# Kernel optimization log

Measured on AMD Instinct MI355X. Metric: run time of the kernel, lower is better.

The kernel has to match this reference:

```python
import jax, jax.numpy as jnp
import numpy as np

B, L, H, N = 50, 1024, 512, 512
DT = 1e-3          # step from source
N_DEQ = 8          # fixed-point iterations for the implicit (DEQ) layer
EPS = 1e-5


def setup_inputs():
    key = jax.random.key(0)
    ks = jax.random.split(key, 8)
    s = lambda k, shape: jax.random.normal(k, shape, jnp.float32) * 0.02
    return dict(
        x=jax.random.normal(ks[0], (B, L, 1), jnp.float32),
        W_emb=s(ks[1], (1, H)), b_emb=jnp.zeros((H,), jnp.float32),
        C_re=s(ks[2], (6, H, N)), C_im=s(ks[3], (6, H, N)),
        D=jnp.ones((6, H), jnp.float32),
        ln_g=jnp.ones((6, H), jnp.float32), ln_b=jnp.zeros((6, H), jnp.float32),
        W_feed=s(ks[4], (H, H)), b_feed=jnp.zeros((H,), jnp.float32),
        W_fc=s(ks[5], (H, 10)), b_fc=jnp.zeros((10,), jnp.float32),
    )


def _kernels(C_re, C_im):
    # S4D-Lin init for A (shared across channels in this untrained reference):
    # A_n = -1/2 + i*pi*n. ZOH discretization with step DT.
    n = jnp.arange(N)
    A = -0.5 + 1j * jnp.pi * n                       # [N]
    dA = jnp.exp(DT * A)                              # [N]
    dB = (dA - 1.0) / A                               # [N] (B = 1)
    l = jnp.arange(L)
    V = jnp.exp(DT * A[:, None] * l[None, :])         # [N, L] Vandermonde dA^l
    C = C_re.astype(jnp.complex64) + 1j * C_im.astype(jnp.complex64)  # [6,H,N]
    K = 2.0 * jnp.real(jnp.einsum('khn,nl->khl', C * dB, V))          # [6,H,L]
    return K.astype(jnp.float32)


def _conv(u, K):
    # causal convolution of u [B,L,H] with per-channel kernel K [H,L]
    Uf = jnp.fft.rfft(u, n=2 * L, axis=1)             # [B, L+1, H]
    Kf = jnp.fft.rfft(K.T, n=2 * L, axis=0)           # [L+1, H]
    y = jnp.fft.irfft(Uf * Kf[None], n=2 * L, axis=1)[:, :L]
    return y


def _ln(x, g, b):
    m = jnp.mean(x, axis=-1, keepdims=True)
    v = jnp.var(x, axis=-1, keepdims=True)
    return (x - m) * jax.lax.rsqrt(v + EPS) * g + b


def _s4d_block(u, K, D, g, b, act, skip):
    v = _ln(u, g, b)
    y = act(_conv(v, K) + v * D)                      # SSM + skip-through D
    return y + u if skip else y


def _deq(x, Ks, Ds, gs, bs, W_feed, b_feed):
    # implicit layer: fixed-point of z = f(z; x), f = 3 stacked S4D blocks
    # + gelu + gelu feedforward, with input injection (skip=False, dropout=0)
    def f(z):
        h = z + x
        for i in range(3):
            h = _s4d_block(h, Ks[i], Ds[i], gs[i], bs[i], jnp.tanh, False)
        h = jax.nn.gelu(h)
        return jax.nn.gelu(h @ W_feed + b_feed)
    z = jnp.zeros_like(x)
    for _ in range(N_DEQ - 1):
        z = f(z)
    z_new = f(z)
    loss = jnp.mean((z_new - z) ** 2)                 # fixed-point residual
    return z_new, loss


def reference(x, W_emb, b_emb, C_re, C_im, D, ln_g, ln_b, W_feed, b_feed, W_fc, b_fc):
    K = _kernels(C_re, C_im)                          # [6,H,L]
    r = x @ W_emb + b_emb                             # [B,L,H]
    y = r
    for i in range(3):                                # 3 explicit S4D blocks
        y = _s4d_block(y, K[i], D[i], ln_g[i], ln_b[i], jnp.tanh, True)
    h, loss = _deq(y, K[3:], D[3:], ln_g[3:], ln_b[3:], W_feed, b_feed)
    logits = jnp.mean(h, axis=1) @ W_fc + b_fc        # [B,10]
    return logits, loss, h, jnp.int32(N_DEQ)
```

## Files before the change

### kernel.cpp

```cpp
#include <hip/hip_runtime.h>
#include <hip/hip_bf16.h>

typedef __hip_bfloat16 bf16;
typedef unsigned short u16;
typedef unsigned int u32;
typedef __attribute__((ext_vector_type(8))) short short8;
typedef __attribute__((ext_vector_type(4))) float f32x4;

#define B_ 50
#define L_ 1024
#define H_ 512
#define N_ 512
#define BL_ 51200
#define HBL_ 26214400
#define KROW_ 1088
#define PI_F 3.14159265358979323846f
#define MARK_BF16 0x3F803F80u
#define KRSW_ 1112
#define CONV_LDS_BYTES 151040

__device__ __forceinline__ float u2f(u16 u){ union{u32 i; float f;} v; v.i = ((u32)u)<<16; return v.f; }
__device__ __forceinline__ u16  f2u(float x){ bf16 b = __float2bfloat16(x); return *(u16*)&b; }

__device__ __forceinline__ float ld_in(const void* p, int i, bool bff){
  if (bff){ u16 v = ((const u16*)p)[i]; union{u32 a; float f;} u; u.a = ((u32)v)<<16; return u.f; }
  return ((const float*)p)[i];
}

__device__ __forceinline__ float gelu_f(float x){
  float t = tanhf(0.7978845608028654f*(x + 0.044715f*x*x*x));
  return 0.5f*x*(1.0f + t);
}

__global__ __launch_bounds__(256) void kV(float* __restrict__ Vre, float* __restrict__ Vim){
  int idx = blockIdx.x*256 + threadIdx.x;
  int n = idx >> 10, l = idx & 1023;
  int ph = (n*l) % 2000;
  float ang = (float)ph * (PI_F/1000.f);
  float mag = expf(-5e-4f*(float)l);
  float s, c;
  sincosf(ang, &s, &c);
  Vre[idx] = mag*c;
  Vim[idx] = mag*s;
}

__global__ __launch_bounds__(256) void kX(const u32* __restrict__ mk,
                                          const void* __restrict__ Cre, const void* __restrict__ Cim,
                                          float* __restrict__ Xre, float* __restrict__ Xim){
  const bool bff = (*mk == MARK_BF16);
  int idx = blockIdx.x*256 + threadIdx.x;
  int n = idx & (N_-1);
  float ar = -0.5f, ai = PI_F*(float)n;
  float ex = expf(-5e-4f);
  float s, c;
  sincosf(1e-3f*ai, &s, &c);
  float dre = ex*c - 1.f;
  float dim = ex*s;
  float inv = 1.f/(ar*ar + ai*ai);
  float dBre = (dre*ar + dim*ai)*inv;
  float dBim = (dim*ar - dre*ai)*inv;
  float cr = ld_in(Cre, idx, bff), ci = ld_in(Cim, idx, bff);
  Xre[idx] = cr*dBre - ci*dBim;
  Xim[idx] = cr*dBim + ci*dBre;
}

__global__ __launch_bounds__(256) void kK(const float* __restrict__ Xre, const float* __restrict__ Xim,
                                          const float* __restrict__ Vre, const float* __restrict__ Vim,
                                          u16* __restrict__ Kbp){
  __shared__ float sxr[16*128], sxi[16*128];
  int kh0 = blockIdx.x*16;
  int l0 = blockIdx.y*512 + threadIdx.x;
  float accA[16], accB[16];
  #pragma unroll
  for (int t=0;t<16;++t){ accA[t]=0.f; accB[t]=0.f; }
  for (int nc=0; nc<4; ++nc){
    if (nc) __syncthreads();
    #pragma unroll
    for (int q=0;q<8;++q){
      int e = q*256 + threadIdx.x;
      int r = e >> 7, c = e & 127;
      sxr[e] = Xre[(kh0+r)*N_ + nc*128 + c];
      sxi[e] = Xim[(kh0+r)*N_ + nc*128 + c];
    }
    __syncthreads();
    for (int n4=0;n4<32;++n4){
      int nb = (nc*128 + n4*4)*L_ + l0;
      float vrA[4], viA[4], vrB[4], viB[4];
      #pragma unroll
      for (int k=0;k<4;++k){
        vrA[k] = Vre[nb + k*L_];       viA[k] = Vim[nb + k*L_];
        vrB[k] = Vre[nb + k*L_ + 256]; viB[k] = Vim[nb + k*L_ + 256];
      }
      #pragma unroll
      for (int t=0;t<16;++t){
        f32x4 xr = *(const f32x4*)&sxr[t*128 + n4*4];
        f32x4 xi = *(const f32x4*)&sxi[t*128 + n4*4];
        float a = accA[t], b = accB[t];
        #pragma unroll
        for (int k=0;k<4;++k){
          a += xr[k]*vrA[k] - xi[k]*viA[k];
          b += xr[k]*vrB[k] - xi[k]*viB[k];
        }
        accA[t] = a; accB[t] = b;
      }
    }
  }
  #pragma unroll
  for (int t=0;t<16;++t){
    Kbp[(kh0+t)*KROW_ + 64 + l0]       = f2u(2.f*accA[t]);
    Kbp[(kh0+t)*KROW_ + 64 + l0 + 256] = f2u(2.f*accB[t]);
  }
  if (blockIdx.y == 0 && threadIdx.x < 64){
    #pragma unroll
    for (int t=0;t<16;++t) Kbp[(kh0+t)*KROW_ + threadIdx.x] = 0;
  }
}

__global__ __launch_bounds__(256) void kWb(const u32* __restrict__ mk,
                                           const void* __restrict__ W, u16* __restrict__ Wbt){
  const bool bff = (*mk == MARK_BF16);
  int idx = blockIdx.x*256 + threadIdx.x;
  int k = idx >> 9, m = idx & 511;
  Wbt[m*512 + k] = f2u(ld_in(W, k*512 + m, bff));
}

__global__ __launch_bounds__(256) void kEmbed(const u32* __restrict__ mk,
                                              const void* __restrict__ x, const void* __restrict__ W,
                                              const void* __restrict__ be, u16* __restrict__ out){
  const bool bff = (*mk == MARK_BF16);
  int t = blockIdx.x*256 + threadIdx.x;
  int e = t*4;
  int h = e / BL_;
  int col = e - h*BL_;
  float w = ld_in(W, h, bff), bb = ld_in(be, h, bff);
  ushort4 o;
  o.x = f2u(ld_in(x, col+0, bff)*w + bb);
  o.y = f2u(ld_in(x, col+1, bff)*w + bb);
  o.z = f2u(ld_in(x, col+2, bff)*w + bb);
  o.w = f2u(ld_in(x, col+3, bff)*w + bb);
  *(ushort4*)(out + e) = o;
}

__global__ __launch_bounds__(256) void kZero(uint4* __restrict__ Z, float* __restrict__ lossAcc){
  int t = blockIdx.x*256 + threadIdx.x;
  Z[t] = make_uint4(0u,0u,0u,0u);
  if (t == 0) *lossAcc = 0.f;
}

__global__ __launch_bounds__(256) void kLN2(const u32* __restrict__ mk,
                                            const u16* __restrict__ U, const u16* __restrict__ U2,
                                            const void* __restrict__ g, const void* __restrict__ bb,
                                            int off, u16* __restrict__ Vout){
  const bool bff = (*mk == MARK_BF16);
  __shared__ float rs[32][64], rq[32][64], ms[64], rr[64], gs[512], bs[512];
  int c8 = threadIdx.x & 7;
  int ty = threadIdx.x >> 3;
  int colb = blockIdx.x*64 + c8*8;
  for (int i = threadIdx.x; i < 512; i += 256){
    gs[i] = ld_in(g, off+i, bff);
    bs[i] = ld_in(bb, off+i, bff);
  }
  float s8[8], q8[8];
  #pragma unroll
  for (int j=0;j<8;++j){ s8[j]=0.f; q8[j]=0.f; }
  for (int p=0;p<16;++p){
    int h = ty + p*32;
    uint4 uv = *(const uint4*)(U + (size_t)h*BL_ + colb);
    const u16* pu = (const u16*)&uv;
    float xv[8];
    #pragma unroll
    for (int j=0;j<8;++j) xv[j] = u2f(pu[j]);
    if (U2){
      uint4 uv2 = *(const uint4*)(U2 + (size_t)h*BL_ + colb);
      const u16* p2 = (const u16*)&uv2;
      #pragma unroll
      for (int j=0;j<8;++j) xv[j] += u2f(p2[j]);
    }
    #pragma unroll
    for (int j=0;j<8;++j){ s8[j] += xv[j]; q8[j] += xv[j]*xv[j]; }
  }
  *(f32x4*)&rs[ty][c8*8]   = (f32x4){s8[0],s8[1],s8[2],s8[3]};
  *(f32x4*)&rs[ty][c8*8+4] = (f32x4){s8[4],s8[5],s8[6],s8[7]};
  *(f32x4*)&rq[ty][c8*8]   = (f32x4){q8[0],q8[1],q8[2],q8[3]};
  *(f32x4*)&rq[ty][c8*8+4] = (f32x4){q8[4],q8[5],q8[6],q8[7]};
  __syncthreads();
  if (threadIdx.x < 64){
    int c = threadIdx.x;
    float st = 0.f, qt = 0.f;
    #pragma unroll 8
    for (int t2=0;t2<32;++t2){ st += rs[t2][c]; qt += rq[t2][c]; }
    float mean = st*(1.f/512.f);
    float var  = qt*(1.f/512.f) - mean*mean;
    ms[c] = mean;
    rr[c] = rsqrtf(var + 1e-5f);
  }
  __syncthreads();
  float mean8[8], rstd8[8];
  #pragma unroll
  for (int j=0;j<8;++j){ mean8[j] = ms[c8*8+j]; rstd8[j] = rr[c8*8+j]; }
  for (int p=0;p<16;++p){
    int h = ty + p*32;
    uint4 uv = *(const uint4*)(U + (size_t)h*BL_ + colb);
    const u16* pu = (const u16*)&uv;
    float xv[8];
    #pragma unroll
    for (int j=0;j<8;++j) xv[j] = u2f(pu[j]);
    if (U2){
      uint4 uv2 = *(const uint4*)(U2 + (size_t)h*BL_ + colb);
      const u16* p2 = (const u16*)&uv2;
      #pragma unroll
      for (int j=0;j<8;++j) xv[j] += u2f(p2[j]);
    }
    float gv = gs[h], bv = bs[h];
    union { uint4 v; u16 s[8]; } ob;
    #pragma unroll
    for (int j=0;j<8;++j) ob.s[j] = f2u((xv[j]-mean8[j])*rstd8[j]*gv + bv);
    *(uint4*)(Vout + (size_t)h*BL_ + colb) = ob.v;
  }
}

__global__ __launch_bounds__(512, 2) void kConvM(const u32* __restrict__ mk,
                                              const u16* __restrict__ V, const u16* __restrict__ Kb,
                                              const void* __restrict__ Dv, int dOff,
                                              const u16* __restrict__ U,
                                              u16* __restrict__ Y, int skip, int doGelu){
  extern __shared__ u16 lds[];
  u16* sV  = lds;
  u16* sKR = lds + 65536;
  u16* sKt = lds + 65536 + 8*KRSW_;
  const bool bff = (*mk == MARK_BF16);
  int h = blockIdx.x;
  int tid = threadIdx.x;
  const u16* Kbh = Kb + h*KROW_;
  for (int s = tid; s < 1088; s += 512) sKt[s] = Kbh[s];
  __syncthreads();
  #pragma unroll
  for (int p = 0; p < 8; ++p){
    for (int s = tid; s < KRSW_; s += 512){
      int idx = 1087 - s - p;
      sKR[p*KRSW_ + s] = (idx >= 0) ? sKt[idx] : (u16)0;
    }
  }
  {
    const u16* Vh = V + (size_t)h*(B_*L_);
    #pragma unroll
    for (int q = 0; q < 16; ++q){
      int chunk = q*512 + tid;
      int r = chunk >> 7;
      int c16 = chunk & 127;
      uint4 dval = *(const uint4*)(Vh + r*L_ + c16*8);
      u32 byte = ((u32)r << 11) + ((u32)c16 << 4);
      byte ^= ((u32)(r & 7) << 4);
      *(uint4*)((char*)sV + byte) = dval;
    }
  }
  __syncthreads();
  int wv = tid >> 6, lane = tid & 63;
  int nl = lane & 15, quad = lane >> 4;
  float Dh = ld_in(Dv, dOff + h, bff);
  #pragma unroll 1
  for (int cc = 0; cc < 2; ++cc){
    int c_out = cc ? (15 - wv) : wv;
    f32x4 acc[4][4];
    #pragma unroll
    for (int mt=0;mt<4;++mt){
      #pragma unroll
      for (int nt=0;nt<4;++nt) acc[mt][nt] = (f32x4){0.f,0.f,0.f,0.f};
    }
    for (int ci = 0; ci <= c_out; ++ci){
      int d = c_out - ci;
      short8 a0[4], a1[4], b0[4], b1[4];
      #pragma unroll
      for (int mt=0;mt<4;++mt){
        int r = mt*16 + nl;
        u32 msk = (u32)(r & 7) << 4;
        u32 base = ((u32)r << 11) + (u32)((ci*64 + quad*8) << 1);
        a0[mt] = *(const short8*)((const char*)sV + (base ^ msk));
        a1[mt] = *(const short8*)((const char*)sV + ((base + 64u) ^ msk));
      }
      #pragma unroll
      for (int nt=0;nt<4;++nt){
        int i = nt*16 + nl;
        int t0 = 1023 - d*64 - i + quad*8;
        const u16* bp = sKR + (t0 & 7)*KRSW_ + (t0 & ~7);
        b0[nt] = *(const short8*)bp;
        b1[nt] = *(const short8*)(bp + 32);
      }
      #pragma unroll
      for (int mt=0;mt<4;++mt){
        #pragma unroll
        for (int nt=0;nt<4;++nt){
          acc[mt][nt] = __builtin_amdgcn_mfma_f32_16x16x32_bf16(a0[mt], b0[nt], acc[mt][nt], 0,0,0);
          acc[mt][nt] = __builtin_amdgcn_mfma_f32_16x16x32_bf16(a1[mt], b1[nt], acc[mt][nt], 0,0,0);
        }
      }
    }
    #pragma unroll
    for (int mt=0;mt<4;++mt){
      #pragma unroll
      for (int reg=0;reg<4;++reg){
        int b = mt*16 + quad*4 + reg;
        if (b < B_){
          #pragma unroll
          for (int nt=0;nt<4;++nt){
            int col = c_out*64 + nt*16 + nl;
            u32 vb = (((u32)b << 11) + ((u32)col << 1)) ^ ((u32)(b & 7) << 4);
            float vv = u2f(*(const u16*)((const char*)sV + vb));
            size_t gi = (size_t)(h*B_ + b)*L_ + col;
            float y = tanhf(acc[mt][nt][reg] + vv*Dh);
            if (skip) y += u2f(U[gi]);
            if (doGelu) y = gelu_f(y);
            Y[gi] = f2u(y);
          }
        }
      }
    }
  }
}

__global__ __launch_bounds__(256) void kTY(const u16* __restrict__ Y, u16* __restrict__ Yt){
  __shared__ u16 st[64][68];
  int n0 = blockIdx.x*64, k0 = blockIdx.y*64;
  int tid = threadIdx.x;
  int r = tid >> 2, q = tid & 3;
  const u16* src = Y + (size_t)(k0 + r)*BL_ + n0 + q*16;
  #pragma unroll
  for (int c=0; c<4; ++c){
    ushort4 v = *(const ushort4*)(src + c*4);
    st[r][q*16 + c*4 + 0] = v.x;
    st[r][q*16 + c*4 + 1] = v.y;
    st[r][q*16 + c*4 + 2] = v.z;
    st[r][q*16 + c*4 + 3] = v.w;
  }
  __syncthreads();
  int i = tid & 63;
  int j0 = tid >> 6;
  for (int jj = j0; jj < 64; jj += 4){
    Yt[(size_t)(n0 + jj)*512 + k0 + i] = st[i][jj];
  }
}

__global__ __launch_bounds__(256) void kFFM(const u32* __restrict__ mk,
                                            const u16* __restrict__ Ytg, const u16* __restrict__ Wbt,
                                            const void* __restrict__ bias, u16* Zout,
                                            const u16* Zold, float* __restrict__ lossAcc, int doLoss){
  const bool bff = (*mk == MARK_BF16);
  int n0g = blockIdx.x*64, m0g = blockIdx.y*64;
  int tid = threadIdx.x;
  __shared__ __align__(16) u16 wa[64*72];
  __shared__ __align__(16) u16 yt[64*72];
  __shared__ float red[256];
  int wv = tid >> 6, lane = tid & 63;
  int nl = lane & 15, quad = lane >> 4;
  int n0 = wv*16;
  f32x4 acc[4];
  #pragma unroll
  for (int mt=0;mt<4;++mt) acc[mt] = (f32x4){0.f,0.f,0.f,0.f};
  int r = tid >> 2, c0 = (tid & 3) * 16;
  for (int kc=0; kc<8; ++kc){
    int k0g = kc*64;
    const u16* wp = Wbt + (m0g + r)*512 + k0g + c0;
    *(uint4*)&wa[r*72 + c0]     = *(const uint4*)wp;
    *(uint4*)&wa[r*72 + c0 + 8] = *(const uint4*)(wp + 8);
    const u16* yp = Ytg + (size_t)(n0g + r)*512 + k0g + c0;
    *(uint4*)&yt[r*72 + c0]     = *(const uint4*)yp;
    *(uint4*)&yt[r*72 + c0 + 8] = *(const uint4*)(yp + 8);
    __syncthreads();
    short8 bf0 = *(const short8*)&yt[(n0 + nl)*72 + quad*8];
    short8 bf1 = *(const short8*)&yt[(n0 + nl)*72 + 32 + quad*8];
    #pragma unroll
    for (int mt=0;mt<4;++mt){
      const u16* row = &wa[(mt*16 + nl)*72];
      short8 a0 = *(const short8*)&row[quad*8];
      short8 a1 = *(const short8*)&row[32 + quad*8];
      acc[mt] = __builtin_amdgcn_mfma_f32_16x16x32_bf16(a0, bf0, acc[mt], 0,0,0);
      acc[mt] = __builtin_amdgcn_mfma_f32_16x16x32_bf16(a1, bf1, acc[mt], 0,0,0);
    }
    __syncthreads();
  }
  float ls = 0.f;
  #pragma unroll
  for (int mt=0;mt<4;++mt){
    #pragma unroll
    for (int reg=0;reg<4;++reg){
      int m = m0g + mt*16 + quad*4 + reg;
      int col = n0g + n0 + nl;
      float val = gelu_f(acc[mt][reg] + ld_in(bias, m, bff));
      size_t zi = (size_t)m*BL_ + col;
      if (doLoss){ float d = val - u2f(Zold[zi]); ls += d*d; }
      Zout[zi] = f2u(val);
    }
  }
  if (doLoss){
    red[tid] = ls;
    __syncthreads();
    for (int off=128; off>0; off>>=1){
      if (tid < off) red[tid] += red[tid+off];
      __syncthreads();
    }
    if (tid==0) atomicAdd(lossAcc, red[0]);
  }
}

__global__ void kScalars(const float* __restrict__ lossAcc, float* __restrict__ outp){
  if (threadIdx.x == 0 && blockIdx.x == 0){
    outp[500] = *lossAcc * (1.f/26214400.f);
    outp[26214901] = 8.0f;
  }
}

__global__ __launch_bounds__(256) void kTrans(const u16* __restrict__ Z, float* __restrict__ out){
  __shared__ u16 st[64][68];
  int b = blockIdx.z, h0 = blockIdx.y*64, l0 = blockIdx.x*64;
  int tid = threadIdx.x;
  int r = tid >> 2, q = tid & 3;
  const u16* src = Z + ((h0+r)*B_ + b)*L_ + l0 + q*16;
  #pragma unroll
  for (int c=0; c<4; ++c){
    ushort4 v = *(const ushort4*)(src + c*4);
    st[r][q*16 + c*4 + 0] = v.x;
    st[r][q*16 + c*4 + 1] = v.y;
    st[r][q*16 + c*4 + 2] = v.z;
    st[r][q*16 + c*4 + 3] = v.w;
  }
  __syncthreads();
  int i = tid & 63;
  int j0 = tid >> 6;
  for (int jj = j0; jj < 64; jj += 4){
    out[(size_t)(b*L_ + l0 + jj)*H_ + h0 + i] = u2f(st[i][jj]);
  }
}

__global__ __launch_bounds__(256) void kMeanL(const u16* __restrict__ Z, float* __restrict__ Hb){
  int lane = threadIdx.x & 63;
  int ridx = blockIdx.x*4 + (threadIdx.x >> 6);
  const u16* row = Z + (size_t)ridx*L_;
  float s = 0.f;
  for (int ii=lane; ii<L_; ii+=64) s += u2f(row[ii]);
  for (int off=32; off>0; off>>=1) s += __shfl_down(s, off, 64);
  if (lane==0){
    int ho = ridx / B_, b = ridx - ho*B_;
    Hb[b*H_ + ho] = s*(1.f/1024.f);
  }
}

__global__ __launch_bounds__(256) void kLogits(const u32* __restrict__ mk,
                                               const float* __restrict__ Hb, const void* __restrict__ Wfc,
                                               const void* __restrict__ bfc, float* __restrict__ outp){
  const bool bff = (*mk == MARK_BF16);
  int t = blockIdx.x*256 + threadIdx.x;
  if (t < 500){
    int b = t/10, c = t - (t/10)*10;
    float s = ld_in(bfc, c, bff);
    for (int ho=0; ho<H_; ++ho) s += Hb[b*H_+ho]*ld_in(Wfc, ho*10+c, bff);
    outp[t] = s;
  }
}

extern "C" void kernel_launch(void* const* d_in, const int* in_sizes, int n_in,
                              void* d_out, int out_size, void* d_ws, size_t ws_size,
                              hipStream_t stream) {
  (void)in_sizes; (void)n_in; (void)out_size; (void)ws_size;
  const void* x      = d_in[0];
  const void* W_emb  = d_in[1];
  const void* b_emb  = d_in[2];
  const void* C_re   = d_in[3];
  const void* C_im   = d_in[4];
  const void* Dp     = d_in[5];
  const void* ln_g   = d_in[6];
  const void* ln_b   = d_in[7];
  const void* W_feed = d_in[8];
  const void* b_feed = d_in[9];
  const void* W_fc   = d_in[10];
  const void* b_fc   = d_in[11];
  const u32* mk = (const u32*)d_in[5];
  float* outp = (float*)d_out;

  static int s_attr = 0;
  if (!s_attr){
    hipFuncSetAttribute(reinterpret_cast<const void*>(kConvM),
                        hipFuncAttributeMaxDynamicSharedMemorySize, CONV_LDS_BYTES);
    s_attr = 1;
  }

  u16* Kbp = (u16*)d_ws;
  u16* Zb  = Kbp + 6*H_*KROW_;
  u16* T1  = Zb + HBL_;
  u16* T2  = T1 + HBL_;
  float* Hbar = (float*)(T2 + HBL_);
  float* lossAcc = Hbar + 25600;
  u16* Wbt = (u16*)(Hbar + 25604);
  u16* X0  = (u16*)d_out;
  u16* Yt  = X0 + HBL_;
  float* Vre = (float*)T1;
  float* Vim = Vre + N_*L_;
  float* Xre = Vim + N_*L_;
  float* Xim = Xre + 6*H_*N_;

  kV<<<2048, 256, 0, stream>>>(Vre, Vim);
  kX<<<6144, 256, 0, stream>>>(mk, C_re, C_im, Xre, Xim);
  kK<<<dim3(192,2), 256, 0, stream>>>(Xre, Xim, Vre, Vim, Kbp);
  kWb<<<1024, 256, 0, stream>>>(mk, W_feed, Wbt);

  kEmbed<<<25600, 256, 0, stream>>>(mk, x, W_emb, b_emb, X0);

  u16* cur = X0;
  u16* nxt = T2;
  for (int i=0;i<3;++i){
    kLN2<<<800,256,0,stream>>>(mk, cur, nullptr, ln_g, ln_b, i*H_, T1);
    kConvM<<<512, 512, CONV_LDS_BYTES, stream>>>(mk, T1, Kbp + i*H_*KROW_, Dp, i*H_, cur, nxt, 1, 0);
    u16* tmp = cur; cur = nxt; nxt = tmp;
  }
  u16* XINJ = cur;
  u16* BT   = nxt;

  kZero<<<12800, 256, 0, stream>>>((uint4*)Zb, lossAcc);
  for (int it=0; it<8; ++it){
    int last = (it == 7);
    kLN2<<<800,256,0,stream>>>(mk, Zb, XINJ, ln_g, ln_b, 3*H_, T1);
    kConvM<<<512, 512, CONV_LDS_BYTES, stream>>>(mk, T1, Kbp + 3*H_*KROW_, Dp, 3*H_, nullptr, BT, 0, 0);
    kLN2<<<800,256,0,stream>>>(mk, BT, nullptr, ln_g, ln_b, 4*H_, T1);
    kConvM<<<512, 512, CONV_LDS_BYTES, stream>>>(mk, T1, Kbp + 4*H_*KROW_, Dp, 4*H_, nullptr, BT, 0, 0);
    kLN2<<<800,256,0,stream>>>(mk, BT, nullptr, ln_g, ln_b, 5*H_, T1);
    kConvM<<<512, 512, CONV_LDS_BYTES, stream>>>(mk, T1, Kbp + 5*H_*KROW_, Dp, 5*H_, nullptr, BT, 0, 1);
    kTY<<<dim3(800,8),256,0,stream>>>(BT, Yt);
    kFFM<<<dim3(800,8),256,0,stream>>>(mk, Yt, Wbt, b_feed, Zb, Zb, lossAcc, last);
  }

  kMeanL<<<6400,256,0,stream>>>(Zb, Hbar);
  kScalars<<<1, 64, 0, stream>>>(lossAcc, outp);
  kTrans<<<dim3(16,8,50),256,0,stream>>>(Zb, outp + 501);
  kLogits<<<2,256,0,stream>>>(mk, Hbar, W_fc, b_fc, outp);
}
```

Baseline: 4.335 ms.

## Fuse transpose into feedforward GEMM, use fast tanh, shrink kernel-gen tiles

Removes the separate kTY transpose and the Yt buffer. The new kFF2 loads a 64-column slab of Y once into LDS, transposes it there, and loops over all 512 output rows while register-prefetching the weight tiles, so Y is read from global memory only once per column block. It also replaces tanhf with an exp-based tanh in the conv epilogue and in gelu, and halves the kK tile height to launch more blocks. The large LDS footprint per block lowers occupancy, and the fast tanh changes numerics slightly.

```diff
diff --git a/kernel.cpp b/kernel.cpp
--- a/kernel.cpp
+++ b/kernel.cpp
@@ -18,6 +18,8 @@
 #define MARK_BF16 0x3F803F80u
 #define KRSW_ 1112
 #define CONV_LDS_BYTES 151040
+#define FF_STR 584
+#define FF2_LDS_BYTES 153600
 
 __device__ __forceinline__ float u2f(u16 u){ union{u32 i; float f;} v; v.i = ((u32)u)<<16; return v.f; }
 __device__ __forceinline__ u16  f2u(float x){ bf16 b = __float2bfloat16(x); return *(u16*)&b; }
@@ -27,8 +29,15 @@
   return ((const float*)p)[i];
 }
 
+__device__ __forceinline__ float tanh_f(float x){
+  float ax = fabsf(x);
+  float e = __expf(2.f*ax);
+  float r = 1.f - 2.f/(e + 1.f);
+  return copysignf(r, x);
+}
+
 __device__ __forceinline__ float gelu_f(float x){
-  float t = tanhf(0.7978845608028654f*(x + 0.044715f*x*x*x));
+  float t = tanh_f(0.7978845608028654f*(x + 0.044715f*x*x*x));
   return 0.5f*x*(1.0f + t);
 }
 
@@ -67,16 +76,16 @@
 __global__ __launch_bounds__(256) void kK(const float* __restrict__ Xre, const float* __restrict__ Xim,
                                           const float* __restrict__ Vre, const float* __restrict__ Vim,
                                           u16* __restrict__ Kbp){
-  __shared__ float sxr[16*128], sxi[16*128];
-  int kh0 = blockIdx.x*16;
+  __shared__ float sxr[8*128], sxi[8*128];
+  int kh0 = blockIdx.x*8;
   int l0 = blockIdx.y*512 + threadIdx.x;
-  float accA[16], accB[16];
+  float accA[8], accB[8];
   #pragma unroll
-  for (int t=0;t<16;++t){ accA[t]=0.f; accB[t]=0.f; }
+  for (int t=0;t<8;++t){ accA[t]=0.f; accB[t]=0.f; }
   for (int nc=0; nc<4; ++nc){
     if (nc) __syncthreads();
     #pragma unroll
-    for (int q=0;q<8;++q){
+    for (int q=0;q<4;++q){
       int e = q*256 + threadIdx.x;
       int r = e >> 7, c = e & 127;
       sxr[e] = Xre[(kh0+r)*N_ + nc*128 + c];
@@ -92,7 +101,7 @@
         vrB[k] = Vre[nb + k*L_ + 256]; viB[k] = Vim[nb + k*L_ + 256];
       }
       #pragma unroll
-      for (int t=0;t<16;++t){
+      for (int t=0;t<8;++t){
         f32x4 xr = *(const f32x4*)&sxr[t*128 + n4*4];
         f32x4 xi = *(const f32x4*)&sxi[t*128 + n4*4];
         float a = accA[t], b = accB[t];
@@ -106,13 +115,13 @@
     }
   }
   #pragma unroll
-  for (int t=0;t<16;++t){
+  for (int t=0;t<8;++t){
     Kbp[(kh0+t)*KROW_ + 64 + l0]       = f2u(2.f*accA[t]);
     Kbp[(kh0+t)*KROW_ + 64 + l0 + 256] = f2u(2.f*accB[t]);
   }
   if (blockIdx.y == 0 && threadIdx.x < 64){
     #pragma unroll
-    for (int t=0;t<16;++t) Kbp[(kh0+t)*KROW_ + threadIdx.x] = 0;
+    for (int t=0;t<8;++t) Kbp[(kh0+t)*KROW_ + threadIdx.x] = 0;
   }
 }
 
@@ -307,7 +316,7 @@
             u32 vb = (((u32)b << 11) + ((u32)col << 1)) ^ ((u32)(b & 7) << 4);
             float vv = u2f(*(const u16*)((const char*)sV + vb));
             size_t gi = (size_t)(h*B_ + b)*L_ + col;
-            float y = tanhf(acc[mt][nt][reg] + vv*Dh);
+            float y = tanh_f(acc[mt][nt][reg] + vv*Dh);
             if (skip) y += u2f(U[gi]);
             if (doGelu) y = gelu_f(y);
             Y[gi] = f2u(y);
@@ -318,83 +327,102 @@
   }
 }
 
-__global__ __launch_bounds__(256) void kTY(const u16* __restrict__ Y, u16* __restrict__ Yt){
-  __shared__ u16 st[64][68];
-  int n0 = blockIdx.x*64, k0 = blockIdx.y*64;
-  int tid = threadIdx.x;
-  int r = tid >> 2, q = tid & 3;
-  const u16* src = Y + (size_t)(k0 + r)*BL_ + n0 + q*16;
-  #pragma unroll
-  for (int c=0; c<4; ++c){
-    ushort4 v = *(const ushort4*)(src + c*4);
-    st[r][q*16 + c*4 + 0] = v.x;
-    st[r][q*16 + c*4 + 1] = v.y;
-    st[r][q*16 + c*4 + 2] = v.z;
-    st[r][q*16 + c*4 + 3] = v.w;
-  }
-  __syncthreads();
-  int i = tid & 63;
-  int j0 = tid >> 6;
-  for (int jj = j0; jj < 64; jj += 4){
-    Yt[(size_t)(n0 + jj)*512 + k0 + i] = st[i][jj];
-  }
-}
-
-__global__ __launch_bounds__(256) void kFFM(const u32* __restrict__ mk,
-                                            const u16* __restrict__ Ytg, const u16* __restrict__ Wbt,
+__global__ __launch_bounds__(512) void kFF2(const u32* __restrict__ mk,
+                                            const u16* __restrict__ Yin, const u16* __restrict__ Wbt,
                                             const void* __restrict__ bias, u16* Zout,
                                             const u16* Zold, float* __restrict__ lossAcc, int doLoss){
-  const bool bff = (*mk == MARK_BF16);
-  int n0g = blockIdx.x*64, m0g = blockIdx.y*64;
+  extern __shared__ u16 lds[];
+  u16* yt = lds;
+  u16* wa = lds + 64*FF_STR;
+  float* sb  = (float*)(lds + 2*64*FF_STR);
+  float* red = sb + 512;
+  const bool bff = (*mk == MARK_BF16);
+  int n0g = blockIdx.x*64;
   int tid = threadIdx.x;
-  __shared__ __align__(16) u16 wa[64*72];
-  __shared__ __align__(16) u16 yt[64*72];
-  __shared__ float red[256];
+
+  if (tid < 512) sb[tid] = ld_in(bias, tid, bff);
+
+  int rW = tid >> 3, kq = tid & 7;
+  uint4 wcur[8], wnxt[8];
+  {
+    const u16* wp = Wbt + (size_t)rW*512 + kq*64;
+    #pragma unroll
+    for (int i=0;i<8;++i) wcur[i] = *(const uint4*)(wp + i*8);
+  }
+
+  {
+    int rY = tid >> 3, q3 = tid & 7;
+    #pragma unroll
+    for (int kc=0;kc<8;++kc){
+      const u16* yp = Yin + (size_t)(kc*64 + rY)*BL_ + n0g + q3*8;
+      uint4 v = *(const uint4*)yp;
+      const u16* pv = (const u16*)&v;
+      #pragma unroll
+      for (int j=0;j<8;++j) yt[(q3*8+j)*FF_STR + kc*72 + rY] = pv[j];
+    }
+  }
+
   int wv = tid >> 6, lane = tid & 63;
   int nl = lane & 15, quad = lane >> 4;
-  int n0 = wv*16;
-  f32x4 acc[4];
-  #pragma unroll
-  for (int mt=0;mt<4;++mt) acc[mt] = (f32x4){0.f,0.f,0.f,0.f};
-  int r = tid >> 2, c0 = (tid & 3) * 16;
-  for (int kc=0; kc<8; ++kc){
-    int k0g = kc*64;
-    const u16* wp = Wbt + (m0g + r)*512 + k0g + c0;
-    *(uint4*)&wa[r*72 + c0]     = *(const uint4*)wp;
-    *(uint4*)&wa[r*72 + c0 + 8] = *(const uint4*)(wp + 8);
-    const u16* yp = Ytg + (size_t)(n0g + r)*512 + k0g + c0;
-    *(uint4*)&yt[r*72 + c0]     = *(const uint4*)yp;
-    *(uint4*)&yt[r*72 + c0 + 8] = *(const uint4*)(yp + 8);
+  int mt = wv >> 1, ntb = (wv & 1)*2;
+  const u16* arow  = wa + (mt*16 + nl)*FF_STR;
+  const u16* brow0 = yt + (ntb*16 + nl)*FF_STR;
+  const u16* brow1 = yt + ((ntb+1)*16 + nl)*FF_STR;
+  float ls = 0.f;
+
+  #pragma unroll 1
+  for (int mc=0; mc<8; ++mc){
+    {
+      u16* wd = wa + rW*FF_STR + kq*72;
+      #pragma unroll
+      for (int i=0;i<8;++i) *(uint4*)(wd + i*8) = wcur[i];
+    }
     __syncthreads();
-    short8 bf0 = *(const short8*)&yt[(n0 + nl)*72 + quad*8];
-    short8 bf1 = *(const short8*)&yt[(n0 + nl)*72 + 32 + quad*8];
-    #pragma unroll
-    for (int mt=0;mt<4;++mt){
-      const u16* row = &wa[(mt*16 + nl)*72];
-      short8 a0 = *(const short8*)&row[quad*8];
-      short8 a1 = *(const short8*)&row[32 + quad*8];
-      acc[mt] = __builtin_amdgcn_mfma_f32_16x16x32_bf16(a0, bf0, acc[mt], 0,0,0);
-      acc[mt] = __builtin_amdgcn_mfma_f32_16x16x32_bf16(a1, bf1, acc[mt], 0,0,0);
+    if (mc < 7){
+      const u16* wp = Wbt + (size_t)(mc+1)*64*512 + (size_t)rW*512 + kq*64;
+      #pragma unroll
+      for (int i=0;i<8;++i) wnxt[i] = *(const uint4*)(wp + i*8);
+    }
+    f32x4 acc0 = (f32x4){0.f,0.f,0.f,0.f};
+    f32x4 acc1 = (f32x4){0.f,0.f,0.f,0.f};
+    #pragma unroll
+    for (int kc=0;kc<8;++kc){
+      int o = kc*72 + quad*8;
+      short8 a0  = *(const short8*)(arow  + o);
+      short8 a1  = *(const short8*)(arow  + o + 32);
+      short8 b00 = *(const short8*)(brow0 + o);
+      short8 b01 = *(const short8*)(brow0 + o + 32);
+      short8 b10 = *(const short8*)(brow1 + o);
+      short8 b11 = *(const short8*)(brow1 + o + 32);
+      acc0 = __builtin_amdgcn_mfma_f32_16x16x32_bf16(a0, b00, acc0, 0,0,0);
+      acc0 = __builtin_amdgcn_mfma_f32_16x16x32_bf16(a1, b01, acc0, 0,0,0);
+      acc1 = __builtin_amdgcn_mfma_f32_16x16x32_bf16(a0, b10, acc1, 0,0,0);
+      acc1 = __builtin_amdgcn_mfma_f32_16x16x32_bf16(a1, b11, acc1, 0,0,0);
+    }
+    #pragma unroll
+    for (int reg=0;reg<4;++reg){
+      int m = mc*64 + mt*16 + quad*4 + reg;
+      float bv = sb[m];
+      int n0 = n0g + ntb*16 + nl;
+      float v0 = gelu_f(acc0[reg] + bv);
+      float v1 = gelu_f(acc1[reg] + bv);
+      size_t z0 = (size_t)m*BL_ + n0;
+      size_t z1 = z0 + 16;
+      if (doLoss){
+        float d0 = v0 - u2f(Zold[z0]); ls += d0*d0;
+        float d1 = v1 - u2f(Zold[z1]); ls += d1*d1;
+      }
+      Zout[z0] = f2u(v0);
+      Zout[z1] = f2u(v1);
     }
     __syncthreads();
-  }
-  float ls = 0.f;
-  #pragma unroll
-  for (int mt=0;mt<4;++mt){
-    #pragma unroll
-    for (int reg=0;reg<4;++reg){
-      int m = m0g + mt*16 + quad*4 + reg;
-      int col = n0g + n0 + nl;
-      float val = gelu_f(acc[mt][reg] + ld_in(bias, m, bff));
-      size_t zi = (size_t)m*BL_ + col;
-      if (doLoss){ float d = val - u2f(Zold[zi]); ls += d*d; }
-      Zout[zi] = f2u(val);
-    }
+    #pragma unroll
+    for (int i=0;i<8;++i) wcur[i] = wnxt[i];
   }
   if (doLoss){
     red[tid] = ls;
     __syncthreads();
-    for (int off=128; off>0; off>>=1){
+    for (int off=256; off>0; off>>=1){
       if (tid < off) red[tid] += red[tid+off];
       __syncthreads();
     }
@@ -480,6 +508,8 @@
   if (!s_attr){
     hipFuncSetAttribute(reinterpret_cast<const void*>(kConvM),
                         hipFuncAttributeMaxDynamicSharedMemorySize, CONV_LDS_BYTES);
+    hipFuncSetAttribute(reinterpret_cast<const void*>(kFF2),
+                        hipFuncAttributeMaxDynamicSharedMemorySize, FF2_LDS_BYTES);
     s_attr = 1;
   }
 
@@ -491,7 +521,6 @@
   float* lossAcc = Hbar + 25600;
   u16* Wbt = (u16*)(Hbar + 25604);
   u16* X0  = (u16*)d_out;
-  u16* Yt  = X0 + HBL_;
   float* Vre = (float*)T1;
   float* Vim = Vre + N_*L_;
   float* Xre = Vim + N_*L_;
@@ -499,7 +528,7 @@
 
   kV<<<2048, 256, 0, stream>>>(Vre, Vim);
   kX<<<6144, 256, 0, stream>>>(mk, C_re, C_im, Xre, Xim);
-  kK<<<dim3(192,2), 256, 0, stream>>>(Xre, Xim, Vre, Vim, Kbp);
+  kK<<<dim3(384,2), 256, 0, stream>>>(Xre, Xim, Vre, Vim, Kbp);
   kWb<<<1024, 256, 0, stream>>>(mk, W_feed, Wbt);
 
   kEmbed<<<25600, 256, 0, stream>>>(mk, x, W_emb, b_emb, X0);
@@ -523,8 +552,7 @@
     kConvM<<<512, 512, CONV_LDS_BYTES, stream>>>(mk, T1, Kbp + 4*H_*KROW_, Dp, 4*H_, nullptr, BT, 0, 0);
     kLN2<<<800,256,0,stream>>>(mk, BT, nullptr, ln_g, ln_b, 5*H_, T1);
     kConvM<<<512, 512, CONV_LDS_BYTES, stream>>>(mk, T1, Kbp + 5*H_*KROW_, Dp, 5*H_, nullptr, BT, 0, 1);
-    kTY<<<dim3(800,8),256,0,stream>>>(BT, Yt);
-    kFFM<<<dim3(800,8),256,0,stream>>>(mk, Yt, Wbt, b_feed, Zb, Zb, lossAcc, last);
+    kFF2<<<800, 512, FF2_LDS_BYTES, stream>>>(mk, BT, Wbt, b_feed, Zb, Zb, lossAcc, last);
   }
 
   kMeanL<<<6400,256,0,stream>>>(Zb, Hbar);
```

New measurement: 5.837 ms. 34.7% more time.
